# Kernel tuning notes

Measured on AMD Instinct MI355X. Metric: run time of the kernel, lower is better.

Reference implementation:

```python
import jax, jax.numpy as jnp
import numpy as np

L, DIN, D, NL = 16384, 256, 768, 8
EPS = 1e-5


def _ln(x, g, b):
    mu = jnp.mean(x, axis=-1, keepdims=True)
    var = jnp.mean(jnp.square(x - mu), axis=-1, keepdims=True)
    return (x - mu) * jax.lax.rsqrt(var + EPS) * g + b


def setup_inputs() -> dict:
    key = jax.random.key(0)
    ks = iter(jax.random.split(key, 24))
    nrm = lambda shape, s=0.02: jax.random.normal(next(ks), shape, jnp.float32) * s
    return {
        "node_features": jax.random.normal(next(ks), (L, DIN), jnp.float32),
        "W_proj": nrm((DIN, D)), "b_proj": jnp.zeros((D,), jnp.float32),
        "ln_s_g": jnp.ones((NL, D), jnp.float32), "ln_s_b": jnp.zeros((NL, D), jnp.float32),
        "W_in": nrm((NL, D, D)), "b_in": jnp.zeros((NL, D), jnp.float32),
        "W_gate": nrm((NL, D, D)), "b_gate": jnp.zeros((NL, D), jnp.float32),
        "W_out": nrm((NL, D, D)), "b_out": jnp.zeros((NL, D), jnp.float32),
        "decay_logit": nrm((NL, D), 0.5),
        "ln_f_g": jnp.ones((NL, D), jnp.float32), "ln_f_b": jnp.zeros((NL, D), jnp.float32),
        "W_ff1": nrm((NL, D, 2 * D)), "b_ff1": jnp.zeros((NL, 2 * D), jnp.float32),
        "W_ff2": nrm((NL, 2 * D, D)), "b_ff2": jnp.zeros((NL, D), jnp.float32),
        "ln_o_g": jnp.ones((D,), jnp.float32), "ln_o_b": jnp.zeros((D,), jnp.float32),
    }


def reference(node_features, W_proj, b_proj, ln_s_g, ln_s_b, W_in, b_in,
              W_gate, b_gate, W_out, b_out, decay_logit, ln_f_g, ln_f_b,
              W_ff1, b_ff1, W_ff2, b_ff2, ln_o_g, ln_o_b):
    x = node_features @ W_proj + b_proj  # [L, D]
    for l in range(NL):
        h = _ln(x, ln_s_g[l], ln_s_b[l])
        u = h @ W_in[l] + b_in[l]                      # [L, D]
        gate = jax.nn.sigmoid(h @ W_gate[l] + b_gate[l])
        decay = jax.nn.sigmoid(decay_logit[l])         # [D]

        def step(state, u_t):
            state = decay * state + u_t
            return state, state

        _, states = jax.lax.scan(step, jnp.zeros((D,), x.dtype), u)  # [L, D]
        x = x + (states * gate) @ W_out[l] + b_out[l]
        hf = _ln(x, ln_f_g[l], ln_f_b[l])
        x = x + jax.nn.silu(hf @ W_ff1[l] + b_ff1[l]) @ W_ff2[l] + b_ff2[l]
    return _ln(x, ln_o_g, ln_o_b)
```

## Files before the change

### kernel.cpp

```cpp
#include <hip/hip_runtime.h>
#include <hip/hip_bf16.h>
#include <math.h>
#include <string.h>

#define L_TOK 16384
#define D_INP 256
#define D_MOD 768
#define D_FF  1536
#define N_LAYER 8
#define S_T 64
#define S_G 256
#define EPSV 1e-5f

typedef short bf16x8 __attribute__((ext_vector_type(8)));
typedef float f32x4 __attribute__((ext_vector_type(4)));
typedef __hip_bfloat16 bf16;
typedef unsigned int u32;
typedef unsigned short u16;

__device__ __forceinline__ float fsigmoid(float z) { return 1.0f / (1.0f + __expf(-z)); }

__device__ __forceinline__ u16 f2bf(float f) {
  __hip_bfloat16 h = __float2bfloat16(f);
  u16 r; memcpy(&r, &h, 2); return r;
}
__device__ __forceinline__ float bf2f(u16 v) {
  u32 x = ((u32)v) << 16; float f; memcpy(&f, &x, 4); return f;
}

__device__ __forceinline__ void glds16(const short* g, short* l) {
  __builtin_amdgcn_global_load_lds(
      (const __attribute__((address_space(1))) unsigned int*)(g),
      (__attribute__((address_space(3))) unsigned int*)(l), 16, 0, 0);
}

__global__ void k_f32_to_bf16v(const float4* __restrict__ src, ushort4* __restrict__ dst, int n4) {
  int i = blockIdx.x * blockDim.x + threadIdx.x;
  if (i < n4) {
    float4 v = src[i];
    ushort4 o; o.x = f2bf(v.x); o.y = f2bf(v.y); o.z = f2bf(v.z); o.w = f2bf(v.w);
    dst[i] = o;
  }
}

__global__ void k_transpose_bf16(const float* __restrict__ src, bf16* __restrict__ dst,
                                 int R, int C, size_t sstride, size_t dstride) {
  __shared__ float tile[32][33];
  const float* s = src + (size_t)blockIdx.z * sstride;
  bf16* d = dst + (size_t)blockIdx.z * dstride;
  int r0 = blockIdx.y * 32, c0 = blockIdx.x * 32;
  int tx = threadIdx.x, ty = threadIdx.y;
#pragma unroll
  for (int i = ty; i < 32; i += 8)
    tile[i][tx] = s[(size_t)(r0 + i) * C + (c0 + tx)];
  __syncthreads();
#pragma unroll
  for (int i = ty; i < 32; i += 8)
    d[(size_t)(c0 + i) * R + (r0 + tx)] = __float2bfloat16(tile[tx][i]);
}

template<bool BF16OUT>
__global__ __launch_bounds__(256) void k_layernorm(const float* __restrict__ x,
    const float* __restrict__ g, const float* __restrict__ b, void* __restrict__ outp) {
  int wv = threadIdx.x >> 6, lane = threadIdx.x & 63;
  int row = blockIdx.x * 4 + wv;
  const float4* xr = (const float4*)(x + (size_t)row * D_MOD);
  float4 v[3];
  float s = 0.f, s2 = 0.f;
#pragma unroll
  for (int j = 0; j < 3; j++) {
    v[j] = xr[j * 64 + lane];
    s  += v[j].x + v[j].y + v[j].z + v[j].w;
    s2 += v[j].x*v[j].x + v[j].y*v[j].y + v[j].z*v[j].z + v[j].w*v[j].w;
  }
#pragma unroll
  for (int o = 32; o >= 1; o >>= 1) {
    s  += __shfl_xor(s, o, 64);
    s2 += __shfl_xor(s2, o, 64);
  }
  float mu = s * (1.0f / (float)D_MOD);
  float var = s2 * (1.0f / (float)D_MOD) - mu * mu;
  float rv = 1.0f / sqrtf(var + EPSV);
  const float4* g4 = (const float4*)g;
  const float4* b4 = (const float4*)b;
#pragma unroll
  for (int j = 0; j < 3; j++) {
    int f = j * 64 + lane;
    float4 gg = g4[f], bb = b4[f], ov;
    ov.x = (v[j].x - mu) * rv * gg.x + bb.x;
    ov.y = (v[j].y - mu) * rv * gg.y + bb.y;
    ov.z = (v[j].z - mu) * rv * gg.z + bb.z;
    ov.w = (v[j].w - mu) * rv * gg.w + bb.w;
    if (BF16OUT) {
      ushort4 o4; o4.x = f2bf(ov.x); o4.y = f2bf(ov.y); o4.z = f2bf(ov.z); o4.w = f2bf(ov.w);
      ((ushort4*)outp)[(size_t)row * 192 + f] = o4;
    } else {
      ((float4*)outp)[(size_t)row * 192 + f] = ov;
    }
  }
}

template<int MODE, bool OUTBF16>
__global__ __launch_bounds__(256, 4) void k_gemm128(
    const short* __restrict__ A, const short* __restrict__ Bt,
    const float* __restrict__ bias, const float* __restrict__ bias2,
    const float* __restrict__ res, void* __restrict__ outp, void* __restrict__ outp2,
    int N, int K, int ncol)
{
  __shared__ short As[2][128 * 32];
  __shared__ short Bs[2][128 * 32];
  const int tid = threadIdx.x;
  const int lane = tid & 63, w = tid >> 6;
  const int wr = w >> 1, wc = w & 1;
  const int l16 = lane & 15, qd = lane >> 4;

  const int b = blockIdx.x;
  const int xcd = b & 7, t = b >> 3;
  const int m0 = (xcd * 16 + t / ncol) * 128;
  const int n0 = (t % ncol) * 128;

  const int sr = lane >> 2, sc = lane & 3;
  const int ar = w * 32 + sr;
  const int acx = sc ^ ((ar >> 1) & 3);
  const short* ag0 = A  + (size_t)(m0 + ar) * K + acx * 8;
  const short* ag1 = ag0 + (size_t)16 * K;
  const short* bg0 = Bt + (size_t)(n0 + ar) * K + acx * 8;
  const short* bg1 = bg0 + (size_t)16 * K;

  const int fo = (qd ^ ((l16 >> 1) & 3)) * 8 + l16 * 32;

  f32x4 acc[4][4];
#pragma unroll
  for (int i = 0; i < 4; i++)
#pragma unroll
    for (int j = 0; j < 4; j++) acc[i][j] = (f32x4){0.f, 0.f, 0.f, 0.f};

  {
    short* a0 = &As[0][w * 1024];
    glds16(ag0, a0); glds16(ag1, a0 + 512);
    short* b0 = &Bs[0][w * 1024];
    glds16(bg0, b0); glds16(bg1, b0 + 512);
  }
  int p = 0;
  for (int k0 = 0; k0 < K; k0 += 32, p ^= 1) {
    __syncthreads();
    if (k0 + 32 < K) {
      short* a0 = &As[p ^ 1][w * 1024];
      glds16(ag0 + k0 + 32, a0); glds16(ag1 + k0 + 32, a0 + 512);
      short* b0 = &Bs[p ^ 1][w * 1024];
      glds16(bg0 + k0 + 32, b0); glds16(bg1 + k0 + 32, b0 + 512);
    }
    const short* afb = &As[p][wr * 2048 + fo];
    const short* bfb = &Bs[p][wc * 2048 + fo];
    bf16x8 af[4], bf[4];
#pragma unroll
    for (int rt = 0; rt < 4; rt++) af[rt] = *(const bf16x8*)(afb + rt * 512);
#pragma unroll
    for (int ct = 0; ct < 4; ct++) bf[ct] = *(const bf16x8*)(bfb + ct * 512);
#pragma unroll
    for (int rt = 0; rt < 4; rt++)
#pragma unroll
      for (int ct = 0; ct < 4; ct++)
        acc[rt][ct] = __builtin_amdgcn_mfma_f32_16x16x32_bf16(af[rt], bf[ct], acc[rt][ct], 0, 0, 0);
  }

  const float* bb = bias;
  void* op = outp;
  int nofs = 0, Nout = N;
  bool sig = false;
  if (MODE == 4) {
    Nout = N >> 1;
    if (n0 >= Nout) { bb = bias2; op = outp2; nofs = Nout; sig = true; }
  }
  const int gmb = m0 + wr * 64 + qd * 4;
  const int gnb = n0 + wc * 64 + l16;
#pragma unroll
  for (int ct = 0; ct < 4; ct++) {
    int gn = gnb + ct * 16;
    float bc = bb[gn - nofs];
#pragma unroll
    for (int rt = 0; rt < 4; rt++) {
#pragma unroll
      for (int r = 0; r < 4; r++) {
        int gm = gmb + rt * 16 + r;
        float vv = acc[rt][ct][r] + bc;
        if (MODE == 2) vv = vv * fsigmoid(vv);
        if (MODE == 4 && sig) vv = fsigmoid(vv);
        size_t oidx = (size_t)gm * Nout + (gn - nofs);
        if (MODE == 3) vv += res[oidx];
        if (OUTBF16) ((bf16*)op)[oidx] = __float2bfloat16(vv);
        else         ((float*)op)[oidx] = vv;
      }
    }
  }
}

__global__ void k_scan_a(const bf16* __restrict__ u, const float* __restrict__ dl,
                         float* __restrict__ clast) {
  int t = threadIdx.x;
  int g = blockIdx.x;
  int d0 = t * 4;
  float dec[4], s[4] = {0.f, 0.f, 0.f, 0.f};
#pragma unroll
  for (int c = 0; c < 4; c++) dec[c] = fsigmoid(dl[d0 + c]);
  const ushort4* up = (const ushort4*)(u + (size_t)g * S_T * D_MOD) + t;
  for (int tt = 0; tt < S_T; tt++) {
    ushort4 uv = up[(size_t)tt * 192];
    s[0] = fmaf(dec[0], s[0], bf2f(uv.x));
    s[1] = fmaf(dec[1], s[1], bf2f(uv.y));
    s[2] = fmaf(dec[2], s[2], bf2f(uv.z));
    s[3] = fmaf(dec[3], s[3], bf2f(uv.w));
  }
#pragma unroll
  for (int c = 0; c < 4; c++) clast[(size_t)g * D_MOD + d0 + c] = s[c];
}

__global__ void k_scan_b(const float* __restrict__ clast, const float* __restrict__ dl,
                         float* __restrict__ carry) {
  int d = threadIdx.x;
  float decay = fsigmoid(dl[d]);
  float aT = decay;
#pragma unroll
  for (int i = 0; i < 6; i++) aT *= aT;
  float c = 0.f;
  for (int g = 0; g < S_G; g++) {
    carry[(size_t)g * D_MOD + d] = c;
    c = fmaf(aT, c, clast[(size_t)g * D_MOD + d]);
  }
}

__global__ void k_scan_c(const bf16* __restrict__ u, const float* __restrict__ dl,
                         const float* __restrict__ carry, bf16* __restrict__ gate_s) {
  int t = threadIdx.x;
  int g = blockIdx.x;
  int d0 = t * 4;
  float dec[4], s[4];
#pragma unroll
  for (int c = 0; c < 4; c++) {
    dec[c] = fsigmoid(dl[d0 + c]);
    s[c] = carry[(size_t)g * D_MOD + d0 + c];
  }
  const ushort4* up = (const ushort4*)(u + (size_t)g * S_T * D_MOD) + t;
  ushort4* gp = (ushort4*)(gate_s + (size_t)g * S_T * D_MOD) + t;
  for (int tt = 0; tt < S_T; tt++) {
    ushort4 uv = up[(size_t)tt * 192];
    ushort4 gv = gp[(size_t)tt * 192];
    s[0] = fmaf(dec[0], s[0], bf2f(uv.x));
    s[1] = fmaf(dec[1], s[1], bf2f(uv.y));
    s[2] = fmaf(dec[2], s[2], bf2f(uv.z));
    s[3] = fmaf(dec[3], s[3], bf2f(uv.w));
    ushort4 ov;
    ov.x = f2bf(s[0] * bf2f(gv.x));
    ov.y = f2bf(s[1] * bf2f(gv.y));
    ov.z = f2bf(s[2] * bf2f(gv.z));
    ov.w = f2bf(s[3] * bf2f(gv.w));
    gp[(size_t)tt * 192] = ov;
  }
}

extern "C" void kernel_launch(void* const* d_in, const int* in_sizes, int n_in,
                              void* d_out, int out_size, void* d_ws, size_t ws_size,
                              hipStream_t stream) {
  const float* nf     = (const float*)d_in[0];
  const float* W_proj = (const float*)d_in[1];
  const float* b_proj = (const float*)d_in[2];
  const float* ln_s_g = (const float*)d_in[3];
  const float* ln_s_b = (const float*)d_in[4];
  const float* W_in   = (const float*)d_in[5];
  const float* b_in   = (const float*)d_in[6];
  const float* W_gate = (const float*)d_in[7];
  const float* b_gate = (const float*)d_in[8];
  const float* W_out  = (const float*)d_in[9];
  const float* b_out  = (const float*)d_in[10];
  const float* dlogit = (const float*)d_in[11];
  const float* ln_f_g = (const float*)d_in[12];
  const float* ln_f_b = (const float*)d_in[13];
  const float* W_ff1  = (const float*)d_in[14];
  const float* b_ff1  = (const float*)d_in[15];
  const float* W_ff2  = (const float*)d_in[16];
  const float* b_ff2  = (const float*)d_in[17];
  const float* ln_o_g = (const float*)d_in[18];
  const float* ln_o_b = (const float*)d_in[19];
  (void)in_sizes; (void)n_in;

  char* ws = (char*)d_ws;
  size_t off = 0;
  auto alloc = [&](size_t bytes) -> char* {
    char* p = ws + off;
    off = (off + bytes + 255) & ~(size_t)255;
    return p;
  };
  const bool big = ws_size >= (195ull << 20);
  const size_t wmul = big ? N_LAYER : 1;

  float* x     = (float*)alloc(sizeof(float) * (size_t)L_TOK * D_MOD);
  bf16*  h     = (bf16*)alloc(2ull * L_TOK * D_MOD);
  char*  ug    = alloc(2ull * L_TOK * D_FF);
  bf16*  u     = (bf16*)ug;
  bf16*  gate  = (bf16*)(ug + 2ull * L_TOK * D_MOD);
  bf16*  tb    = (bf16*)ug;
  bf16*  nfb   = (bf16*)ug;
  bf16*  WprojT= (bf16*)alloc(2ull * D_INP * D_MOD);
  bf16*  WigT  = (bf16*)alloc(2ull * wmul * (2 * D_MOD) * D_MOD);
  bf16*  WoT   = (bf16*)alloc(2ull * wmul * D_MOD * D_MOD);
  bf16*  Wff1T = (bf16*)alloc(2ull * wmul * D_MOD * D_FF);
  bf16*  Wff2T = (bf16*)alloc(2ull * wmul * D_FF * D_MOD);
  float* clast = (float*)alloc(sizeof(float) * (size_t)S_G * D_MOD);
  float* carry = (float*)alloc(sizeof(float) * (size_t)S_G * D_MOD);

  const size_t DD = (size_t)D_MOD * D_MOD, DF = (size_t)D_MOD * D_FF;
  dim3 tb32(32, 8);
  k_f32_to_bf16v<<<(L_TOK * D_INP / 4 + 255) / 256, 256, 0, stream>>>(
      (const float4*)nf, (ushort4*)nfb, L_TOK * D_INP / 4);
  k_transpose_bf16<<<dim3(D_MOD / 32, D_INP / 32, 1), tb32, 0, stream>>>(
      W_proj, WprojT, D_INP, D_MOD, 0, 0);
  if (big) {
    k_transpose_bf16<<<dim3(D_MOD / 32, D_MOD / 32, N_LAYER), tb32, 0, stream>>>(
        W_in,   WigT,       D_MOD, D_MOD, DD, 2 * DD);
    k_transpose_bf16<<<dim3(D_MOD / 32, D_MOD / 32, N_LAYER), tb32, 0, stream>>>(
        W_gate, WigT + DD,  D_MOD, D_MOD, DD, 2 * DD);
    k_transpose_bf16<<<dim3(D_MOD / 32, D_MOD / 32, N_LAYER), tb32, 0, stream>>>(
        W_out,  WoT,        D_MOD, D_MOD, DD, DD);
    k_transpose_bf16<<<dim3(D_FF / 32,  D_MOD / 32, N_LAYER), tb32, 0, stream>>>(
        W_ff1,  Wff1T,      D_MOD, D_FF,  DF, DF);
    k_transpose_bf16<<<dim3(D_MOD / 32, D_FF / 32,  N_LAYER), tb32, 0, stream>>>(
        W_ff2,  Wff2T,      D_FF,  D_MOD, DF, DF);
  }

  k_gemm128<0, false><<<128 * 6, 256, 0, stream>>>(
      (const short*)nfb, (const short*)WprojT, b_proj, nullptr, nullptr, x, nullptr,
      D_MOD, D_INP, 6);

  for (int l = 0; l < N_LAYER; l++) {
    const bf16 *wigT, *woT, *wf1T, *wf2T;
    if (big) {
      wigT = WigT  + (size_t)l * 2 * DD;
      woT  = WoT   + (size_t)l * DD;
      wf1T = Wff1T + (size_t)l * DF;
      wf2T = Wff2T + (size_t)l * DF;
    } else {
      k_transpose_bf16<<<dim3(D_MOD / 32, D_MOD / 32, 1), tb32, 0, stream>>>(
          W_in + (size_t)l * DD, WigT, D_MOD, D_MOD, 0, 0);
      k_transpose_bf16<<<dim3(D_MOD / 32, D_MOD / 32, 1), tb32, 0, stream>>>(
          W_gate + (size_t)l * DD, WigT + DD, D_MOD, D_MOD, 0, 0);
      k_transpose_bf16<<<dim3(D_MOD / 32, D_MOD / 32, 1), tb32, 0, stream>>>(
          W_out + (size_t)l * DD, WoT, D_MOD, D_MOD, 0, 0);
      k_transpose_bf16<<<dim3(D_FF / 32, D_MOD / 32, 1), tb32, 0, stream>>>(
          W_ff1 + (size_t)l * DF, Wff1T, D_MOD, D_FF, 0, 0);
      k_transpose_bf16<<<dim3(D_MOD / 32, D_FF / 32, 1), tb32, 0, stream>>>(
          W_ff2 + (size_t)l * DF, Wff2T, D_FF, D_MOD, 0, 0);
      wigT = WigT; woT = WoT; wf1T = Wff1T; wf2T = Wff2T;
    }

    k_layernorm<true><<<L_TOK / 4, 256, 0, stream>>>(x, ln_s_g + l * D_MOD, ln_s_b + l * D_MOD, h);
    k_gemm128<4, true><<<128 * 12, 256, 0, stream>>>(
        (const short*)h, (const short*)wigT, b_in + l * D_MOD, b_gate + l * D_MOD,
        nullptr, u, gate, 2 * D_MOD, D_MOD, 12);
    k_scan_a<<<S_G, 192, 0, stream>>>(u, dlogit + l * D_MOD, clast);
    k_scan_b<<<1, D_MOD, 0, stream>>>(clast, dlogit + l * D_MOD, carry);
    k_scan_c<<<S_G, 192, 0, stream>>>(u, dlogit + l * D_MOD, carry, gate);
    k_gemm128<3, false><<<128 * 6, 256, 0, stream>>>(
        (const short*)gate, (const short*)woT, b_out + l * D_MOD, nullptr, x, x, nullptr,
        D_MOD, D_MOD, 6);
    k_layernorm<true><<<L_TOK / 4, 256, 0, stream>>>(x, ln_f_g + l * D_MOD, ln_f_b + l * D_MOD, h);
    k_gemm128<2, true><<<128 * 12, 256, 0, stream>>>(
        (const short*)h, (const short*)wf1T, b_ff1 + l * D_FF, nullptr, nullptr, tb, nullptr,
        D_FF, D_MOD, 12);
    k_gemm128<3, false><<<128 * 6, 256, 0, stream>>>(
        (const short*)tb, (const short*)wf2T, b_ff2 + l * D_MOD, nullptr, x, x, nullptr,
        D_MOD, D_FF, 6);
  }

  k_layernorm<false><<<L_TOK / 4, 256, 0, stream>>>(x, ln_o_g, ln_o_b, d_out);
}
```

Measured before the change: 2.556 ms.

## Triple-buffer GEMM shared-memory tiles with explicit vmcnt waits

Moves the bf16 GEMM main loop from double to triple buffering of the A/B LDS tiles, keeping two tiles of global-to-LDS loads in flight ahead of compute. Explicit s_waitcnt vmcnt/lgkmcnt plus barriers replace the plain __syncthreads. The goal is to hide global load latency better. In exchange it uses 50% more LDS per block, which can lower occupancy, and it issues redundant wrap-around loads in the last iterations so the vmcnt count stays constant.

```diff
diff --git a/kernel.cpp b/kernel.cpp
--- a/kernel.cpp
+++ b/kernel.cpp
@@ -107,8 +107,8 @@
     const float* __restrict__ res, void* __restrict__ outp, void* __restrict__ outp2,
     int N, int K, int ncol)
 {
-  __shared__ short As[2][128 * 32];
-  __shared__ short Bs[2][128 * 32];
+  __shared__ short As[3][128 * 32];
+  __shared__ short Bs[3][128 * 32];
   const int tid = threadIdx.x;
   const int lane = tid & 63, w = tid >> 6;
   const int wr = w >> 1, wc = w & 1;
@@ -135,33 +135,36 @@
 #pragma unroll
     for (int j = 0; j < 4; j++) acc[i][j] = (f32x4){0.f, 0.f, 0.f, 0.f};
 
-  {
-    short* a0 = &As[0][w * 1024];
-    glds16(ag0, a0); glds16(ag1, a0 + 512);
-    short* b0 = &Bs[0][w * 1024];
-    glds16(bg0, b0); glds16(bg1, b0 + 512);
-  }
+  const int NI = K >> 5;
+  auto issue = [&](int ti, int st) {
+    const size_t ko = (size_t)ti * 32;
+    short* a0 = &As[st][w * 1024];
+    glds16(ag0 + ko, a0); glds16(ag1 + ko, a0 + 512);
+    short* b0 = &Bs[st][w * 1024];
+    glds16(bg0 + ko, b0); glds16(bg1 + ko, b0 + 512);
+  };
+  issue(0, 0); issue(1, 1); issue(2, 2);
+
   int p = 0;
-  for (int k0 = 0; k0 < K; k0 += 32, p ^= 1) {
-    __syncthreads();
-    if (k0 + 32 < K) {
-      short* a0 = &As[p ^ 1][w * 1024];
-      glds16(ag0 + k0 + 32, a0); glds16(ag1 + k0 + 32, a0 + 512);
-      short* b0 = &Bs[p ^ 1][w * 1024];
-      glds16(bg0 + k0 + 32, b0); glds16(bg1 + k0 + 32, b0 + 512);
-    }
+  for (int i = 0; i < NI; i++) {
+    asm volatile("s_waitcnt vmcnt(8)\n\ts_barrier" ::: "memory");
     const short* afb = &As[p][wr * 2048 + fo];
     const short* bfb = &Bs[p][wc * 2048 + fo];
-    bf16x8 af[4], bf[4];
+    bf16x8 af[4], bfr[4];
 #pragma unroll
     for (int rt = 0; rt < 4; rt++) af[rt] = *(const bf16x8*)(afb + rt * 512);
 #pragma unroll
-    for (int ct = 0; ct < 4; ct++) bf[ct] = *(const bf16x8*)(bfb + ct * 512);
+    for (int ct = 0; ct < 4; ct++) bfr[ct] = *(const bf16x8*)(bfb + ct * 512);
 #pragma unroll
     for (int rt = 0; rt < 4; rt++)
 #pragma unroll
       for (int ct = 0; ct < 4; ct++)
-        acc[rt][ct] = __builtin_amdgcn_mfma_f32_16x16x32_bf16(af[rt], bf[ct], acc[rt][ct], 0, 0, 0);
+        acc[rt][ct] = __builtin_amdgcn_mfma_f32_16x16x32_bf16(af[rt], bfr[ct], acc[rt][ct], 0, 0, 0);
+    asm volatile("s_waitcnt lgkmcnt(0)\n\ts_barrier" ::: "memory");
+    int nt = i + 3;
+    if (nt >= NI) nt -= NI;
+    issue(nt, p);
+    p = (p == 2) ? 0 : p + 1;
   }
 
   const float* bb = bias;
```

Result: slower. 2.710 ms (+6.0%).

## Fold LayerNorm into GEMM weights and epilogues, store residual in bf16

Applied to the files above, without the earlier changes.

Removes the standalone layernorm kernels. The LN gain is folded into the transposed weights, and the mean/variance correction is applied in the GEMM epilogue using per-row sum and sum-of-squares statistics. Those statistics are accumulated with atomics by the preceding residual GEMM. The residual stream x is now kept in bf16 instead of fp32, which halves residual traffic but costs accuracy, and the E[x²]-mu² variance form can cancel badly. Atomic stats accumulation and the folded-weight reductions add contention and a memset of the stats buffers.

```diff
diff --git a/kernel.cpp b/kernel.cpp
--- a/kernel.cpp
+++ b/kernel.cpp
@@ -43,72 +43,57 @@
   }
 }
 
-__global__ void k_transpose_bf16(const float* __restrict__ src, bf16* __restrict__ dst,
-                                 int R, int C, size_t sstride, size_t dstride) {
+template<bool FOLD>
+__global__ void k_transpose_fold(const float* __restrict__ src, bf16* __restrict__ dst,
+                                 int R, int C, size_t sstride, size_t dstride,
+                                 const float* __restrict__ gv, const float* __restrict__ bv,
+                                 float* __restrict__ wacc, float* __restrict__ bacc,
+                                 int vstride) {
   __shared__ float tile[32][33];
-  const float* s = src + (size_t)blockIdx.z * sstride;
-  bf16* d = dst + (size_t)blockIdx.z * dstride;
+  int z = blockIdx.z;
+  const float* s = src + (size_t)z * sstride;
+  bf16* d = dst + (size_t)z * dstride;
   int r0 = blockIdx.y * 32, c0 = blockIdx.x * 32;
   int tx = threadIdx.x, ty = threadIdx.y;
 #pragma unroll
   for (int i = ty; i < 32; i += 8)
     tile[i][tx] = s[(size_t)(r0 + i) * C + (c0 + tx)];
   __syncthreads();
-#pragma unroll
-  for (int i = ty; i < 32; i += 8)
-    d[(size_t)(c0 + i) * R + (r0 + tx)] = __float2bfloat16(tile[tx][i]);
-}
-
-template<bool BF16OUT>
-__global__ __launch_bounds__(256) void k_layernorm(const float* __restrict__ x,
-    const float* __restrict__ g, const float* __restrict__ b, void* __restrict__ outp) {
-  int wv = threadIdx.x >> 6, lane = threadIdx.x & 63;
-  int row = blockIdx.x * 4 + wv;
-  const float4* xr = (const float4*)(x + (size_t)row * D_MOD);
-  float4 v[3];
-  float s = 0.f, s2 = 0.f;
-#pragma unroll
-  for (int j = 0; j < 3; j++) {
-    v[j] = xr[j * 64 + lane];
-    s  += v[j].x + v[j].y + v[j].z + v[j].w;
-    s2 += v[j].x*v[j].x + v[j].y*v[j].y + v[j].z*v[j].z + v[j].w*v[j].w;
-  }
-#pragma unroll
-  for (int o = 32; o >= 1; o >>= 1) {
-    s  += __shfl_xor(s, o, 64);
-    s2 += __shfl_xor(s2, o, 64);
-  }
-  float mu = s * (1.0f / (float)D_MOD);
-  float var = s2 * (1.0f / (float)D_MOD) - mu * mu;
-  float rv = 1.0f / sqrtf(var + EPSV);
-  const float4* g4 = (const float4*)g;
-  const float4* b4 = (const float4*)b;
-#pragma unroll
-  for (int j = 0; j < 3; j++) {
-    int f = j * 64 + lane;
-    float4 gg = g4[f], bb = b4[f], ov;
-    ov.x = (v[j].x - mu) * rv * gg.x + bb.x;
-    ov.y = (v[j].y - mu) * rv * gg.y + bb.y;
-    ov.z = (v[j].z - mu) * rv * gg.z + bb.z;
-    ov.w = (v[j].w - mu) * rv * gg.w + bb.w;
-    if (BF16OUT) {
-      ushort4 o4; o4.x = f2bf(ov.x); o4.y = f2bf(ov.y); o4.z = f2bf(ov.z); o4.w = f2bf(ov.w);
-      ((ushort4*)outp)[(size_t)row * 192 + f] = o4;
-    } else {
-      ((float4*)outp)[(size_t)row * 192 + f] = ov;
+  float gk = 1.0f;
+  if (FOLD) gk = gv[(size_t)z * R + r0 + tx];
+#pragma unroll
+  for (int i = ty; i < 32; i += 8) {
+    float val = tile[tx][i];
+    if (FOLD) val *= gk;
+    d[(size_t)(c0 + i) * R + (r0 + tx)] = __float2bfloat16(val);
+  }
+  if (FOLD && ty == 0) {
+    const float* gz = gv + (size_t)z * R + r0;
+    const float* bz = bv + (size_t)z * R + r0;
+    float s1 = 0.f, s2 = 0.f;
+#pragma unroll 8
+    for (int j = 0; j < 32; j++) {
+      float wv = tile[j][tx];
+      s1 += gz[j] * wv;
+      s2 += bz[j] * wv;
     }
-  }
-}
-
-template<int MODE, bool OUTBF16>
+    atomicAdd(&wacc[(size_t)z * vstride + c0 + tx], s1);
+    atomicAdd(&bacc[(size_t)z * vstride + c0 + tx], s2);
+  }
+}
+
+template<int MODE, bool LNFOLD, bool STATS>
 __global__ __launch_bounds__(256, 4) void k_gemm128(
     const short* __restrict__ A, const short* __restrict__ Bt,
     const float* __restrict__ bias, const float* __restrict__ bias2,
-    const float* __restrict__ res, void* __restrict__ outp, void* __restrict__ outp2,
+    const float* __restrict__ wvec, const float* __restrict__ bvec,
+    const float* __restrict__ stats_in, float* __restrict__ stats_out,
+    u16* __restrict__ res, u16* __restrict__ outp, u16* __restrict__ outp2,
     int N, int K, int ncol)
 {
   __shared__ short As[2][128 * 32];
   __shared__ short Bs[2][128 * 32];
+  __shared__ float s_mu[128], s_rv[128];
   const int tid = threadIdx.x;
   const int lane = tid & 63, w = tid >> 6;
   const int wr = w >> 1, wc = w & 1;
@@ -140,6 +125,14 @@
     glds16(ag0, a0); glds16(ag1, a0 + 512);
     short* b0 = &Bs[0][w * 1024];
     glds16(bg0, b0); glds16(bg1, b0 + 512);
+  }
+  if (LNFOLD && tid < 128) {
+    float sv  = stats_in[2 * (m0 + tid)];
+    float sq  = stats_in[2 * (m0 + tid) + 1];
+    float mu  = sv * (1.0f / (float)D_MOD);
+    float var = sq * (1.0f / (float)D_MOD) - mu * mu;
+    s_mu[tid] = mu;
+    s_rv[tid] = 1.0f / sqrtf(var + EPSV);
   }
   int p = 0;
   for (int k0 = 0; k0 < K; k0 += 32, p ^= 1) {
@@ -152,20 +145,20 @@
     }
     const short* afb = &As[p][wr * 2048 + fo];
     const short* bfb = &Bs[p][wc * 2048 + fo];
-    bf16x8 af[4], bf[4];
+    bf16x8 af[4], bfr[4];
 #pragma unroll
     for (int rt = 0; rt < 4; rt++) af[rt] = *(const bf16x8*)(afb + rt * 512);
 #pragma unroll
-    for (int ct = 0; ct < 4; ct++) bf[ct] = *(const bf16x8*)(bfb + ct * 512);
+    for (int ct = 0; ct < 4; ct++) bfr[ct] = *(const bf16x8*)(bfb + ct * 512);
 #pragma unroll
     for (int rt = 0; rt < 4; rt++)
 #pragma unroll
       for (int ct = 0; ct < 4; ct++)
-        acc[rt][ct] = __builtin_amdgcn_mfma_f32_16x16x32_bf16(af[rt], bf[ct], acc[rt][ct], 0, 0, 0);
+        acc[rt][ct] = __builtin_amdgcn_mfma_f32_16x16x32_bf16(af[rt], bfr[ct], acc[rt][ct], 0, 0, 0);
   }
 
   const float* bb = bias;
-  void* op = outp;
+  u16* op = outp;
   int nofs = 0, Nout = N;
   bool sig = false;
   if (MODE == 4) {
@@ -174,22 +167,45 @@
   }
   const int gmb = m0 + wr * 64 + qd * 4;
   const int gnb = n0 + wc * 64 + l16;
+  float bc[4], wv4[4], bv4[4];
 #pragma unroll
   for (int ct = 0; ct < 4; ct++) {
     int gn = gnb + ct * 16;
-    float bc = bb[gn - nofs];
-#pragma unroll
-    for (int rt = 0; rt < 4; rt++) {
-#pragma unroll
-      for (int r = 0; r < 4; r++) {
-        int gm = gmb + rt * 16 + r;
-        float vv = acc[rt][ct][r] + bc;
+    bc[ct] = bb[gn - nofs];
+    if (LNFOLD) { wv4[ct] = wvec[gn]; bv4[ct] = bvec[gn]; }
+  }
+#pragma unroll
+  for (int rt = 0; rt < 4; rt++) {
+#pragma unroll
+    for (int r = 0; r < 4; r++) {
+      const int gm = gmb + rt * 16 + r;
+      float mu = 0.f, rv = 0.f;
+      if (LNFOLD) { mu = s_mu[gm - m0]; rv = s_rv[gm - m0]; }
+      float ps = 0.f, ps2 = 0.f;
+#pragma unroll
+      for (int ct = 0; ct < 4; ct++) {
+        int gn = gnb + ct * 16;
+        float vv = acc[rt][ct][r];
+        if (LNFOLD) vv = rv * vv - rv * mu * wv4[ct] + bv4[ct] + bc[ct];
+        else        vv += bc[ct];
         if (MODE == 2) vv = vv * fsigmoid(vv);
         if (MODE == 4 && sig) vv = fsigmoid(vv);
         size_t oidx = (size_t)gm * Nout + (gn - nofs);
-        if (MODE == 3) vv += res[oidx];
-        if (OUTBF16) ((bf16*)op)[oidx] = __float2bfloat16(vv);
-        else         ((float*)op)[oidx] = vv;
+        if (MODE == 3) vv += bf2f(res[oidx]);
+        u16 rb = f2bf(vv);
+        op[oidx] = rb;
+        if (STATS) { float fv = bf2f(rb); ps += fv; ps2 += fv * fv; }
+      }
+      if (STATS) {
+#pragma unroll
+        for (int o = 1; o < 16; o <<= 1) {
+          ps  += __shfl_xor(ps, o, 64);
+          ps2 += __shfl_xor(ps2, o, 64);
+        }
+        if (l16 == 0) {
+          atomicAdd(&stats_out[2 * gm], ps);
+          atomicAdd(&stats_out[2 * gm + 1], ps2);
+        }
       }
     }
   }
@@ -255,6 +271,32 @@
     ov.z = f2bf(s[2] * bf2f(gv.z));
     ov.w = f2bf(s[3] * bf2f(gv.w));
     gp[(size_t)tt * 192] = ov;
+  }
+}
+
+__global__ __launch_bounds__(256) void k_ln_final(const u16* __restrict__ x,
+    const float* __restrict__ stats, const float* __restrict__ g,
+    const float* __restrict__ b, float* __restrict__ outp) {
+  int wv = threadIdx.x >> 6, lane = threadIdx.x & 63;
+  int row = blockIdx.x * 4 + wv;
+  float sv = stats[2 * row], sq = stats[2 * row + 1];
+  float mu = sv * (1.0f / (float)D_MOD);
+  float var = sq * (1.0f / (float)D_MOD) - mu * mu;
+  float rv = 1.0f / sqrtf(var + EPSV);
+  const ushort4* xr = (const ushort4*)(x + (size_t)row * D_MOD);
+  const float4* g4 = (const float4*)g;
+  const float4* b4 = (const float4*)b;
+  float4* o4 = (float4*)(outp + (size_t)row * D_MOD);
+#pragma unroll
+  for (int j = 0; j < 3; j++) {
+    int f = j * 64 + lane;
+    ushort4 xv = xr[f];
+    float4 gg = g4[f], bb = b4[f], ov;
+    ov.x = (bf2f(xv.x) - mu) * rv * gg.x + bb.x;
+    ov.y = (bf2f(xv.y) - mu) * rv * gg.y + bb.y;
+    ov.z = (bf2f(xv.z) - mu) * rv * gg.z + bb.z;
+    ov.w = (bf2f(xv.w) - mu) * rv * gg.w + bb.w;
+    o4[f] = ov;
   }
 }
 
@@ -290,16 +332,15 @@
     off = (off + bytes + 255) & ~(size_t)255;
     return p;
   };
-  const bool big = ws_size >= (195ull << 20);
+  const bool big = ws_size >= (160ull << 20);
   const size_t wmul = big ? N_LAYER : 1;
 
-  float* x     = (float*)alloc(sizeof(float) * (size_t)L_TOK * D_MOD);
-  bf16*  h     = (bf16*)alloc(2ull * L_TOK * D_MOD);
+  u16*   x     = (u16*)alloc(2ull * L_TOK * D_MOD);
   char*  ug    = alloc(2ull * L_TOK * D_FF);
-  bf16*  u     = (bf16*)ug;
-  bf16*  gate  = (bf16*)(ug + 2ull * L_TOK * D_MOD);
-  bf16*  tb    = (bf16*)ug;
-  bf16*  nfb   = (bf16*)ug;
+  u16*   u     = (u16*)ug;
+  u16*   gate  = (u16*)(ug + 2ull * L_TOK * D_MOD);
+  u16*   tb    = (u16*)ug;
+  u16*   nfb   = (u16*)ug;
   bf16*  WprojT= (bf16*)alloc(2ull * D_INP * D_MOD);
   bf16*  WigT  = (bf16*)alloc(2ull * wmul * (2 * D_MOD) * D_MOD);
   bf16*  WoT   = (bf16*)alloc(2ull * wmul * D_MOD * D_MOD);
@@ -307,29 +348,38 @@
   bf16*  Wff2T = (bf16*)alloc(2ull * wmul * D_FF * D_MOD);
   float* clast = (float*)alloc(sizeof(float) * (size_t)S_G * D_MOD);
   float* carry = (float*)alloc(sizeof(float) * (size_t)S_G * D_MOD);
+  char*  zbase = alloc(0);
+  float* stats = (float*)alloc(sizeof(float) * 17ull * L_TOK * 2);
+  float* wvig  = (float*)alloc(sizeof(float) * N_LAYER * 2 * D_MOD);
+  float* bvig  = (float*)alloc(sizeof(float) * N_LAYER * 2 * D_MOD);
+  float* wvf1  = (float*)alloc(sizeof(float) * N_LAYER * D_FF);
+  float* bvf1  = (float*)alloc(sizeof(float) * N_LAYER * D_FF);
+  size_t zbytes = (size_t)((char*)ws + off - zbase);
+  hipMemsetAsync(zbase, 0, zbytes, stream);
 
   const size_t DD = (size_t)D_MOD * D_MOD, DF = (size_t)D_MOD * D_FF;
+  auto statslot = [&](int s) { return stats + (size_t)s * L_TOK * 2; };
   dim3 tb32(32, 8);
   k_f32_to_bf16v<<<(L_TOK * D_INP / 4 + 255) / 256, 256, 0, stream>>>(
       (const float4*)nf, (ushort4*)nfb, L_TOK * D_INP / 4);
-  k_transpose_bf16<<<dim3(D_MOD / 32, D_INP / 32, 1), tb32, 0, stream>>>(
-      W_proj, WprojT, D_INP, D_MOD, 0, 0);
+  k_transpose_fold<false><<<dim3(D_MOD / 32, D_INP / 32, 1), tb32, 0, stream>>>(
+      W_proj, WprojT, D_INP, D_MOD, 0, 0, nullptr, nullptr, nullptr, nullptr, 0);
   if (big) {
-    k_transpose_bf16<<<dim3(D_MOD / 32, D_MOD / 32, N_LAYER), tb32, 0, stream>>>(
-        W_in,   WigT,       D_MOD, D_MOD, DD, 2 * DD);
-    k_transpose_bf16<<<dim3(D_MOD / 32, D_MOD / 32, N_LAYER), tb32, 0, stream>>>(
-        W_gate, WigT + DD,  D_MOD, D_MOD, DD, 2 * DD);
-    k_transpose_bf16<<<dim3(D_MOD / 32, D_MOD / 32, N_LAYER), tb32, 0, stream>>>(
-        W_out,  WoT,        D_MOD, D_MOD, DD, DD);
-    k_transpose_bf16<<<dim3(D_FF / 32,  D_MOD / 32, N_LAYER), tb32, 0, stream>>>(
-        W_ff1,  Wff1T,      D_MOD, D_FF,  DF, DF);
-    k_transpose_bf16<<<dim3(D_MOD / 32, D_FF / 32,  N_LAYER), tb32, 0, stream>>>(
-        W_ff2,  Wff2T,      D_FF,  D_MOD, DF, DF);
-  }
-
-  k_gemm128<0, false><<<128 * 6, 256, 0, stream>>>(
-      (const short*)nfb, (const short*)WprojT, b_proj, nullptr, nullptr, x, nullptr,
-      D_MOD, D_INP, 6);
+    k_transpose_fold<true><<<dim3(D_MOD / 32, D_MOD / 32, N_LAYER), tb32, 0, stream>>>(
+        W_in,   WigT,      D_MOD, D_MOD, DD, 2 * DD, ln_s_g, ln_s_b, wvig,       bvig,       2 * D_MOD);
+    k_transpose_fold<true><<<dim3(D_MOD / 32, D_MOD / 32, N_LAYER), tb32, 0, stream>>>(
+        W_gate, WigT + DD, D_MOD, D_MOD, DD, 2 * DD, ln_s_g, ln_s_b, wvig + D_MOD, bvig + D_MOD, 2 * D_MOD);
+    k_transpose_fold<false><<<dim3(D_MOD / 32, D_MOD / 32, N_LAYER), tb32, 0, stream>>>(
+        W_out,  WoT,       D_MOD, D_MOD, DD, DD, nullptr, nullptr, nullptr, nullptr, 0);
+    k_transpose_fold<true><<<dim3(D_FF / 32,  D_MOD / 32, N_LAYER), tb32, 0, stream>>>(
+        W_ff1,  Wff1T,     D_MOD, D_FF,  DF, DF, ln_f_g, ln_f_b, wvf1, bvf1, D_FF);
+    k_transpose_fold<false><<<dim3(D_MOD / 32, D_FF / 32,  N_LAYER), tb32, 0, stream>>>(
+        W_ff2,  Wff2T,     D_FF,  D_MOD, DF, DF, nullptr, nullptr, nullptr, nullptr, 0);
+  }
+
+  k_gemm128<0, false, true><<<128 * 6, 256, 0, stream>>>(
+      (const short*)nfb, (const short*)WprojT, b_proj, nullptr, nullptr, nullptr,
+      nullptr, statslot(0), nullptr, x, nullptr, D_MOD, D_INP, 6);
 
   for (int l = 0; l < N_LAYER; l++) {
     const bf16 *wigT, *woT, *wf1T, *wf2T;
@@ -339,37 +389,40 @@
       wf1T = Wff1T + (size_t)l * DF;
       wf2T = Wff2T + (size_t)l * DF;
     } else {
-      k_transpose_bf16<<<dim3(D_MOD / 32, D_MOD / 32, 1), tb32, 0, stream>>>(
-          W_in + (size_t)l * DD, WigT, D_MOD, D_MOD, 0, 0);
-      k_transpose_bf16<<<dim3(D_MOD / 32, D_MOD / 32, 1), tb32, 0, stream>>>(
-          W_gate + (size_t)l * DD, WigT + DD, D_MOD, D_MOD, 0, 0);
-      k_transpose_bf16<<<dim3(D_MOD / 32, D_MOD / 32, 1), tb32, 0, stream>>>(
-          W_out + (size_t)l * DD, WoT, D_MOD, D_MOD, 0, 0);
-      k_transpose_bf16<<<dim3(D_FF / 32, D_MOD / 32, 1), tb32, 0, stream>>>(
-          W_ff1 + (size_t)l * DF, Wff1T, D_MOD, D_FF, 0, 0);
-      k_transpose_bf16<<<dim3(D_MOD / 32, D_FF / 32, 1), tb32, 0, stream>>>(
-          W_ff2 + (size_t)l * DF, Wff2T, D_FF, D_MOD, 0, 0);
+      k_transpose_fold<true><<<dim3(D_MOD / 32, D_MOD / 32, 1), tb32, 0, stream>>>(
+          W_in + (size_t)l * DD, WigT, D_MOD, D_MOD, 0, 0,
+          ln_s_g + l * D_MOD, ln_s_b + l * D_MOD, wvig + (size_t)l * 2 * D_MOD, bvig + (size_t)l * 2 * D_MOD, 0);
+      k_transpose_fold<true><<<dim3(D_MOD / 32, D_MOD / 32, 1), tb32, 0, stream>>>(
+          W_gate + (size_t)l * DD, WigT + DD, D_MOD, D_MOD, 0, 0,
+          ln_s_g + l * D_MOD, ln_s_b + l * D_MOD, wvig + (size_t)l * 2 * D_MOD + D_MOD, bvig + (size_t)l * 2 * D_MOD + D_MOD, 0);
+      k_transpose_fold<false><<<dim3(D_MOD / 32, D_MOD / 32, 1), tb32, 0, stream>>>(
+          W_out + (size_t)l * DD, WoT, D_MOD, D_MOD, 0, 0, nullptr, nullptr, nullptr, nullptr, 0);
+      k_transpose_fold<true><<<dim3(D_FF / 32, D_MOD / 32, 1), tb32, 0, stream>>>(
+          W_ff1 + (size_t)l * DF, Wff1T, D_MOD, D_FF, 0, 0,
+          ln_f_g + l * D_MOD, ln_f_b + l * D_MOD, wvf1 + (size_t)l * D_FF, bvf1 + (size_t)l * D_FF, 0);
+      k_transpose_fold<false><<<dim3(D_MOD / 32, D_FF / 32, 1), tb32, 0, stream>>>(
+          W_ff2 + (size_t)l * DF, Wff2T, D_FF, D_MOD, 0, 0, nullptr, nullptr, nullptr, nullptr, 0);
       wigT = WigT; woT = WoT; wf1T = Wff1T; wf2T = Wff2T;
     }
 
-    k_layernorm<true><<<L_TOK / 4, 256, 0, stream>>>(x, ln_s_g + l * D_MOD, ln_s_b + l * D_MOD, h);
-    k_gemm128<4, true><<<128 * 12, 256, 0, stream>>>(
-        (const short*)h, (const short*)wigT, b_in + l * D_MOD, b_gate + l * D_MOD,
-        nullptr, u, gate, 2 * D_MOD, D_MOD, 12);
-    k_scan_a<<<S_G, 192, 0, stream>>>(u, dlogit + l * D_MOD, clast);
+    k_gemm128<4, true, false><<<128 * 12, 256, 0, stream>>>(
+        (const short*)x, (const short*)wigT, b_in + l * D_MOD, b_gate + l * D_MOD,
+        wvig + (size_t)l * 2 * D_MOD, bvig + (size_t)l * 2 * D_MOD,
+        statslot(2 * l), nullptr, nullptr, u, gate, 2 * D_MOD, D_MOD, 12);
+    k_scan_a<<<S_G, 192, 0, stream>>>((const bf16*)u, dlogit + l * D_MOD, clast);
     k_scan_b<<<1, D_MOD, 0, stream>>>(clast, dlogit + l * D_MOD, carry);
-    k_scan_c<<<S_G, 192, 0, stream>>>(u, dlogit + l * D_MOD, carry, gate);
-    k_gemm128<3, false><<<128 * 6, 256, 0, stream>>>(
-        (const short*)gate, (const short*)woT, b_out + l * D_MOD, nullptr, x, x, nullptr,
-        D_MOD, D_MOD, 6);
-    k_layernorm<true><<<L_TOK / 4, 256, 0, stream>>>(x, ln_f_g + l * D_MOD, ln_f_b + l * D_MOD, h);
-    k_gemm128<2, true><<<128 * 12, 256, 0, stream>>>(
-        (const short*)h, (const short*)wf1T, b_ff1 + l * D_FF, nullptr, nullptr, tb, nullptr,
-        D_FF, D_MOD, 12);
-    k_gemm128<3, false><<<128 * 6, 256, 0, stream>>>(
-        (const short*)tb, (const short*)wf2T, b_ff2 + l * D_MOD, nullptr, x, x, nullptr,
-        D_MOD, D_FF, 6);
-  }
-
-  k_layernorm<false><<<L_TOK / 4, 256, 0, stream>>>(x, ln_o_g, ln_o_b, d_out);
-}
+    k_scan_c<<<S_G, 192, 0, stream>>>((const bf16*)u, dlogit + l * D_MOD, carry, (bf16*)gate);
+    k_gemm128<3, false, true><<<128 * 6, 256, 0, stream>>>(
+        (const short*)gate, (const short*)woT, b_out + l * D_MOD, nullptr, nullptr, nullptr,
+        nullptr, statslot(2 * l + 1), x, x, nullptr, D_MOD, D_MOD, 6);
+    k_gemm128<2, true, false><<<128 * 12, 256, 0, stream>>>(
+        (const short*)x, (const short*)wf1T, b_ff1 + l * D_FF, nullptr,
+        wvf1 + (size_t)l * D_FF, bvf1 + (size_t)l * D_FF,
+        statslot(2 * l + 1), nullptr, nullptr, tb, nullptr, D_FF, D_MOD, 12);
+    k_gemm128<3, false, true><<<128 * 6, 256, 0, stream>>>(
+        (const short*)tb, (const short*)wf2T, b_ff2 + l * D_MOD, nullptr, nullptr, nullptr,
+        nullptr, statslot(2 * l + 2), x, x, nullptr, D_MOD, D_FF, 6);
+  }
+
+  k_ln_final<<<L_TOK / 4, 256, 0, stream>>>(x, statslot(2 * N_LAYER), ln_o_g, ln_o_b, (float*)d_out);
+}
```

Result: faster. 2.277 ms (-10.9%).
